# Performance work log

Measured on AMD Instinct MI355X. Metric: run time of the kernel, lower is better.

## Reference

```python
import jax, jax.numpy as jnp
import numpy as np

B, S, D = 8, 2048, 768
SCALE = jnp.sqrt(jnp.float32(D))


def setup_inputs() -> dict:
    key = jax.random.key(0)
    ks = jax.random.split(key, 9)
    sd = 1.0 / np.sqrt(D)
    return {
        "x": jax.random.normal(ks[0], (B, S, D), jnp.float32),
        "Wq": jax.random.normal(ks[1], (D, D), jnp.float32) * sd,
        "bq": jax.random.normal(ks[2], (D,), jnp.float32) * sd,
        "Wk": jax.random.normal(ks[3], (D, D), jnp.float32) * sd,
        "bk": jax.random.normal(ks[4], (D,), jnp.float32) * sd,
        "Wv": jax.random.normal(ks[5], (D, D), jnp.float32) * sd,
        "bv": jax.random.normal(ks[6], (D,), jnp.float32) * sd,
        "Wp": jax.random.normal(ks[7], (D, D), jnp.float32) * sd,
        "bp": jax.random.normal(ks[8], (D,), jnp.float32) * sd,
    }


def reference(x, Wq, bq, Wk, bk, Wv, bv, Wp, bp):
    # Linear layers: y = x @ W^T + b (torch nn.Linear convention)
    Q = jnp.einsum("bsd,ed->bse", x, Wq) + bq
    K = jnp.einsum("bsd,ed->bse", x, Wk) + bk
    V = jnp.einsum("bsd,ed->bse", x, Wv) + bv
    # Full attention matrix (no head split in original module)
    alpha = jnp.einsum("bqd,bkd->bqk", Q, K) / SCALE  # [B,S,S]
    alpha = jax.nn.softmax(alpha, axis=-1)
    # dropout is identity in eval mode
    out = jnp.einsum("bqk,bkd->bqd", alpha, V)
    out = jnp.einsum("bsd,ed->bse", out, Wp) + bp
    return out
```

## Files before the change

### kernel.cpp

```cpp
#include <hip/hip_runtime.h>
#include <stdint.h>


typedef __attribute__((ext_vector_type(8))) short short8;
typedef __attribute__((ext_vector_type(4))) float f32x4;

typedef const __attribute__((address_space(1))) void gvoid_t;
typedef __attribute__((address_space(3))) void lvoid_t;

__device__ __forceinline__ float b2f(unsigned short u) {
  union { unsigned int u; float f; } v;
  v.u = ((unsigned int)u) << 16;
  return v.f;
}
__device__ __forceinline__ unsigned short f2b(float f) {
  union { float f; unsigned int u; } v; v.f = f;
  unsigned int u = v.u;
  return (unsigned short)((u + 0x7fffu + ((u >> 16) & 1u)) >> 16);
}

struct Cvt9 {
  const void* s[9];
  unsigned short* d[9];
  long long n8[9];
  long long total8;
};

__global__ __launch_bounds__(256) void convert_inputs(Cvt9 C) {
  long long g = (long long)blockIdx.x * 256 + threadIdx.x;
  if (g >= C.total8) return;
  int s = 0;
  long long off = g;
  while (off >= C.n8[s]) { off -= C.n8[s]; ++s; }
  const float* sf = (const float*)C.s[s] + off * 8;
  unsigned short* dp = C.d[s] + off * 8;
  float4 a = ((const float4*)sf)[0];
  float4 b = ((const float4*)sf)[1];
  uint4 o;
  o.x = (unsigned int)f2b(a.x) | ((unsigned int)f2b(a.y) << 16);
  o.y = (unsigned int)f2b(a.z) | ((unsigned int)f2b(a.w) << 16);
  o.z = (unsigned int)f2b(b.x) | ((unsigned int)f2b(b.y) << 16);
  o.w = (unsigned int)f2b(b.z) | ((unsigned int)f2b(b.w) << 16);
  *(uint4*)dp = o;
}

__device__ __forceinline__ void gemm_core(
    const unsigned short* __restrict__ Ab, const unsigned short* __restrict__ Bb,
    int lda, int ldb, int K, int m0, int n0,
    unsigned short* As, unsigned short* Bs, f32x4 (&acc)[4][4])
{
  const int t    = threadIdx.x;
  const int w    = t >> 6;
  const int lane = t & 63;
  const int lo   = lane & 15;
  const int quad = lane >> 4;
  const int wr   = w >> 1;
  const int wc   = w & 1;
  const int srow  = t >> 2;
  const int sq    = ((t & 3) - ((t >> 3) & 3)) & 3;
  const int skoff = sq * 8;
  const int rq    = ((quad + (lo >> 1)) & 3) * 8;

  for (int k0 = 0; k0 < K; k0 += 64) {
#pragma unroll
    for (int c = 0; c < 2; ++c) {
#pragma unroll
      for (int r = 0; r < 2; ++r) {
        const unsigned short* ga = Ab + (size_t)(m0 + r * 64 + srow) * lda + (k0 + c * 32 + skoff);
        __builtin_amdgcn_global_load_lds((gvoid_t*)ga, (lvoid_t*)(As + c * 4096 + r * 2048 + w * 512), 16, 0, 0);
        const unsigned short* gb = Bb + (size_t)(n0 + r * 64 + srow) * ldb + (k0 + c * 32 + skoff);
        __builtin_amdgcn_global_load_lds((gvoid_t*)gb, (lvoid_t*)(Bs + c * 4096 + r * 2048 + w * 512), 16, 0, 0);
      }
    }
    __syncthreads();

#pragma unroll
    for (int c = 0; c < 2; ++c) {
      short8 af[4], bf[4];
#pragma unroll
      for (int i = 0; i < 4; ++i)
        af[i] = *(const short8*)(As + c * 4096 + wr * 2048 + (i * 16 + lo) * 32 + rq);
#pragma unroll
      for (int j = 0; j < 4; ++j)
        bf[j] = *(const short8*)(Bs + c * 4096 + wc * 2048 + (j * 16 + lo) * 32 + rq);

#pragma unroll
      for (int i = 0; i < 4; ++i)
#pragma unroll
        for (int j = 0; j < 4; ++j)
          acc[i][j] = __builtin_amdgcn_mfma_f32_16x16x32_bf16(af[i], bf[j], acc[i][j], 0, 0, 0);
    }
    __syncthreads();
  }
}

__device__ __forceinline__ void tile_to_lds(
    unsigned short* Ls, f32x4 (&acc)[4][4], int mode,
    const unsigned short* bias_n0, const float* rlrow, float scale)
{
  const int t = threadIdx.x;
  const int w = t >> 6, lane = t & 63;
  const int lo = lane & 15, quad = lane >> 4, wr = w >> 1, wc = w & 1;
#pragma unroll
  for (int j = 0; j < 4; ++j) {
    const int ct = wc * 64 + j * 16 + lo;
    const float bv = (mode == 0) ? b2f(bias_n0[ct]) : 0.f;
#pragma unroll
    for (int i = 0; i < 4; ++i) {
      const int rt = wr * 64 + i * 16 + quad * 4;
#pragma unroll
      for (int r = 0; r < 4; ++r) {
        float v = acc[i][j][r];
        if (mode == 0)      v += bv;
        else if (mode == 2) v = __expf(fminf(v * scale, 30.f));
        else                v *= __builtin_amdgcn_rcpf(rlrow[rt + r]);
        Ls[(rt + r) * 136 + ct] = f2b(v);
      }
    }
  }
  __syncthreads();
}

__device__ __forceinline__ void lds_to_global_bf16(
    const unsigned short* Ls, unsigned short* Cg, int ldc)
{
  const int t = threadIdx.x;
  const int cr = t >> 4, cc = (t & 15) * 8;
#pragma unroll
  for (int r0 = 0; r0 < 128; r0 += 16) {
    uint4 v = *(const uint4*)(Ls + (r0 + cr) * 136 + cc);
    *(uint4*)(Cg + (size_t)(r0 + cr) * ldc + cc) = v;
  }
}

__global__ __launch_bounds__(256, 2) void qkv_k(
    const unsigned short* __restrict__ xb,
    const unsigned short* __restrict__ Wq, const unsigned short* __restrict__ bq,
    const unsigned short* __restrict__ Wk, const unsigned short* __restrict__ bk,
    const unsigned short* __restrict__ Wv, const unsigned short* __restrict__ bv,
    unsigned short* __restrict__ qb, unsigned short* __restrict__ kb,
    unsigned short* __restrict__ vt)
{
  __shared__ unsigned short smem[17408];
  const int sel = blockIdx.y / 6;
  const int n0  = (blockIdx.y % 6) * 128;
  const int m0  = blockIdx.x * 128;

  const unsigned short* W;
  const unsigned short* bi;
  if (sel == 0)      { W = Wq; bi = bq; }
  else if (sel == 1) { W = Wk; bi = bk; }
  else               { W = Wv; bi = bv; }

  f32x4 acc[4][4] = {};
  gemm_core(xb, W, 768, 768, 768, m0, n0, smem, smem + 8192, acc);

  const int t = threadIdx.x;
  const int w = t >> 6, lane = t & 63;
  const int lo = lane & 15, quad = lane >> 4, wr = w >> 1, wc = w & 1;

  if (sel < 2) {
    tile_to_lds(smem, acc, 0, bi + n0, nullptr, 0.f);
    unsigned short* dst = (sel == 0) ? qb : kb;
    lds_to_global_bf16(smem, dst + (size_t)m0 * 768 + n0, 768);
    return;
  }

  unsigned short* Ls = smem;
#pragma unroll
  for (int i = 0; i < 4; ++i) {
    const int rt = wr * 64 + i * 16 + quad * 4;
#pragma unroll
    for (int j = 0; j < 4; ++j) {
      const int ct = wc * 64 + j * 16 + lo;
      const float bvv = b2f(bi[n0 + ct]);
      ushort4 pk;
      pk.x = f2b(acc[i][j][0] + bvv);
      pk.y = f2b(acc[i][j][1] + bvv);
      pk.z = f2b(acc[i][j][2] + bvv);
      pk.w = f2b(acc[i][j][3] + bvv);
      *(ushort4*)(Ls + ct * 136 + rt) = pk;
    }
  }
  __syncthreads();
  const int bb  = m0 >> 11;
  const int sin = m0 & 2047;
  unsigned short* Cb = vt + (size_t)bb * (768 * 2048);
#pragma unroll
  for (int e0 = 0; e0 < 128; e0 += 16) {
    const int et = e0 + (t >> 4);
    const int st = (t & 15) * 8;
    uint4 val = *(const uint4*)(Ls + et * 136 + st);
    *(uint4*)(Cb + (size_t)(n0 + et) * 2048 + (sin + st)) = val;
  }
}

__global__ __launch_bounds__(256, 2) void score_k(
    const unsigned short* __restrict__ Q, const unsigned short* __restrict__ Kb,
    unsigned short* __restrict__ E, float* __restrict__ rl, float scale)
{
  __shared__ unsigned short smem[17408];
  const int m0 = blockIdx.x * 128, n0 = blockIdx.y * 128, bz = blockIdx.z;

  f32x4 acc[4][4] = {};
  gemm_core(Q + (size_t)bz * 1572864, Kb + (size_t)bz * 1572864,
            768, 768, 768, m0, n0, smem, smem + 8192, acc);

  tile_to_lds(smem, acc, 2, nullptr, nullptr, scale);
  lds_to_global_bf16(smem, E + (size_t)bz * 4194304 + (size_t)m0 * 2048 + n0, 2048);

  const int t = threadIdx.x;
  const int row = t >> 1, half = t & 1;
  const unsigned short* lr = smem + row * 136 + half * 64;
  float s = 0.f;
#pragma unroll
  for (int q8 = 0; q8 < 8; ++q8) {
    uint4 v = *(const uint4*)(lr + q8 * 8);
    unsigned int uu[4] = {v.x, v.y, v.z, v.w};
#pragma unroll
    for (int c = 0; c < 4; ++c)
      s += b2f((unsigned short)(uu[c] & 0xffffu)) + b2f((unsigned short)(uu[c] >> 16));
  }
  s += __shfl_xor(s, 1);
  if (half == 0) atomicAdd(rl + bz * 2048 + m0 + row, s);
}

__global__ __launch_bounds__(256, 2) void pv_k(
    const unsigned short* __restrict__ E, const unsigned short* __restrict__ Vt,
    const float* __restrict__ rl, unsigned short* __restrict__ attn)
{
  __shared__ unsigned short smem[17408];
  const int m0 = blockIdx.x * 128, n0 = blockIdx.y * 128, bz = blockIdx.z;

  f32x4 acc[4][4] = {};
  gemm_core(E + (size_t)bz * 4194304, Vt + (size_t)bz * 1572864,
            2048, 2048, 2048, m0, n0, smem, smem + 8192, acc);

  tile_to_lds(smem, acc, 3, nullptr, rl + bz * 2048 + m0, 0.f);
  lds_to_global_bf16(smem, attn + (size_t)bz * 1572864 + (size_t)m0 * 768 + n0, 768);
}

__global__ __launch_bounds__(256, 2) void out_k(
    const unsigned short* __restrict__ attn,
    const unsigned short* __restrict__ Wp, const unsigned short* __restrict__ bp,
    float* __restrict__ Of)
{
  __shared__ unsigned short smem[17408];
  const int m0 = blockIdx.x * 128, n0 = blockIdx.y * 128;

  f32x4 acc[4][4] = {};
  gemm_core(attn, Wp, 768, 768, 768, m0, n0, smem, smem + 8192, acc);

  const int t = threadIdx.x;
  const int w = t >> 6, lane = t & 63;
  const int lo = lane & 15, quad = lane >> 4, wr = w >> 1, wc = w & 1;
  float* Lf = (float*)smem;
#pragma unroll
  for (int h = 0; h < 2; ++h) {
    __syncthreads();
    if (wc == h) {
#pragma unroll
      for (int j = 0; j < 4; ++j) {
        const int cl = j * 16 + lo;
        const float bvv = b2f(bp[n0 + h * 64 + cl]);
#pragma unroll
        for (int i = 0; i < 4; ++i) {
          const int rt = wr * 64 + i * 16 + quad * 4;
#pragma unroll
          for (int r = 0; r < 4; ++r)
            Lf[(rt + r) * 68 + cl] = acc[i][j][r] + bvv;
        }
      }
    }
    __syncthreads();
    const int cr = t >> 4, cc = (t & 15) * 4;
#pragma unroll
    for (int r0 = 0; r0 < 128; r0 += 16) {
      float4 v = *(const float4*)(Lf + (r0 + cr) * 68 + cc);
      *(float4*)(Of + (size_t)(m0 + r0 + cr) * 768 + n0 + h * 64 + cc) = v;
    }
  }
}

extern "C" void kernel_launch(void* const* d_in, const int* in_sizes, int n_in,
                              void* d_out, int out_size, void* d_ws, size_t ws_size,
                              hipStream_t stream) {
  (void)in_sizes; (void)n_in; (void)out_size; (void)ws_size;

  char* ws = (char*)d_ws;
  float* rl    = (float*)(ws + 4096);
  unsigned short* wcv = (unsigned short*)(ws + ((size_t)1 << 20));
  unsigned short* qb  = (unsigned short*)(ws + ((size_t)8  << 20));
  unsigned short* kb  = (unsigned short*)(ws + ((size_t)32 << 20));
  unsigned short* vt  = (unsigned short*)(ws + ((size_t)56 << 20));
  unsigned short* eb  = (unsigned short*)(ws + ((size_t)80 << 20));
  unsigned short* xb  = eb;
  unsigned short* attn = qb;

  unsigned short* wqb = wcv;
  unsigned short* bqb = wcv + 589824;
  unsigned short* wkb = wcv + 590592;
  unsigned short* bkb = wcv + 1180416;
  unsigned short* wvb = wcv + 1181184;
  unsigned short* bvb = wcv + 1771008;
  unsigned short* wpb = wcv + 1771776;
  unsigned short* bpb = wcv + 2361600;

  const float inv_scale = 0.036084391824351615f;
  dim3 blk(256);

  Cvt9 cv;
  cv.s[0] = d_in[0]; cv.d[0] = xb;  cv.n8[0] = 12582912 / 8;
  cv.s[1] = d_in[1]; cv.d[1] = wqb; cv.n8[1] = 589824 / 8;
  cv.s[2] = d_in[2]; cv.d[2] = bqb; cv.n8[2] = 768 / 8;
  cv.s[3] = d_in[3]; cv.d[3] = wkb; cv.n8[3] = 589824 / 8;
  cv.s[4] = d_in[4]; cv.d[4] = bkb; cv.n8[4] = 768 / 8;
  cv.s[5] = d_in[5]; cv.d[5] = wvb; cv.n8[5] = 589824 / 8;
  cv.s[6] = d_in[6]; cv.d[6] = bvb; cv.n8[6] = 768 / 8;
  cv.s[7] = d_in[7]; cv.d[7] = wpb; cv.n8[7] = 589824 / 8;
  cv.s[8] = d_in[8]; cv.d[8] = bpb; cv.n8[8] = 768 / 8;
  cv.total8 = (12582912 + 4 * (589824 + 768)) / 8;
  convert_inputs<<<(unsigned)((cv.total8 + 255) / 256), blk, 0, stream>>>(cv);

  hipMemsetAsync(rl, 0, 16384 * sizeof(float), stream);

  qkv_k<<<dim3(128, 18, 1), blk, 0, stream>>>(xb, wqb, bqb, wkb, bkb, wvb, bvb, qb, kb, vt);

  score_k<<<dim3(16, 16, 8), blk, 0, stream>>>(qb, kb, eb, rl, inv_scale);

  pv_k<<<dim3(16, 6, 8), blk, 0, stream>>>(eb, vt, rl, attn);

  out_k<<<dim3(128, 6, 1), blk, 0, stream>>>(attn, wpb, bpb, (float*)d_out);
}
```

Before: 354.7 us.

## Replace 128x128 GEMM core with double-buffered 256x256 pipelined MFMA kernel

Replaces the shared GEMM core with a 256x256-tile, 512-thread kernel. It double-buffers 64-wide K slices in LDS using XOR-swizzled direct-to-LDS loads, and interleaves prefetch of the next slices with MFMA quarter-blocks through explicit vmcnt waits, barriers and setprio. All four GEMM kernels, the epilogues and the launch grids are rewritten for the larger tile, with epilogues staged in two halves through LDS. The aim is more operand reuse per byte loaded and hiding global-load latency behind compute. In exchange it uses 128KB of LDS and many more accumulator registers per block, so occupancy drops, and the smaller grids (e.g. 192 blocks for pv_k) may leave CUs underused.

```diff
diff --git a/kernel.cpp b/kernel.cpp
--- a/kernel.cpp
+++ b/kernel.cpp
@@ -44,96 +44,147 @@
   *(uint4*)dp = o;
 }
 
-__device__ __forceinline__ void gemm_core(
-    const unsigned short* __restrict__ Ab, const unsigned short* __restrict__ Bb,
-    int lda, int ldb, int K, int m0, int n0,
-    unsigned short* As, unsigned short* Bs, f32x4 (&acc)[4][4])
+__device__ __forceinline__ void gemm256(
+    const unsigned short* __restrict__ Ag,
+    const unsigned short* __restrict__ Bg,
+    const int lda, const int ldb, const int NT,
+    unsigned short* lds, f32x4 (&acc)[8][4])
 {
   const int t    = threadIdx.x;
   const int w    = t >> 6;
   const int lane = t & 63;
   const int lo   = lane & 15;
   const int quad = lane >> 4;
-  const int wr   = w >> 1;
-  const int wc   = w & 1;
-  const int srow  = t >> 2;
-  const int sq    = ((t & 3) - ((t >> 3) & 3)) & 3;
-  const int skoff = sq * 8;
-  const int rq    = ((quad + (lo >> 1)) & 3) * 8;
-
-  for (int k0 = 0; k0 < K; k0 += 64) {
-#pragma unroll
-    for (int c = 0; c < 2; ++c) {
-#pragma unroll
-      for (int r = 0; r < 2; ++r) {
-        const unsigned short* ga = Ab + (size_t)(m0 + r * 64 + srow) * lda + (k0 + c * 32 + skoff);
-        __builtin_amdgcn_global_load_lds((gvoid_t*)ga, (lvoid_t*)(As + c * 4096 + r * 2048 + w * 512), 16, 0, 0);
-        const unsigned short* gb = Bb + (size_t)(n0 + r * 64 + srow) * ldb + (k0 + c * 32 + skoff);
-        __builtin_amdgcn_global_load_lds((gvoid_t*)gb, (lvoid_t*)(Bs + c * 4096 + r * 2048 + w * 512), 16, 0, 0);
+  const int wr   = w >> 2;
+  const int wcn  = w & 3;
+  const int swz  = ((t & 7) ^ ((t >> 3) & 7)) << 3;
+  const int wslot = w * 512;
+  const int sl0  = (quad ^ (lo & 7)) << 3;
+  const int sl1  = ((4 + quad) ^ (lo & 7)) << 3;
+  const unsigned short* pA = lds + wr * 8192 + lo * 64;
+  const unsigned short* pB = lds + 16384 + (wcn >> 1) * 8192 + ((wcn & 1) * 64 + lo) * 64;
+
+  short8 af[4][2], bf0[2][2], bf1[2][2];
+
+#define STG(gb, ld, kt, q, reg)                                                   \
+  __builtin_amdgcn_global_load_lds(                                               \
+      (gvoid_t*)((gb) + (size_t)((q) * 64 + (t >> 3)) * (ld) + (kt) * 64 + swz),  \
+      (lvoid_t*)((reg) + wslot), 16, 0, 0)
+#define SA02(kt) { unsigned short* r_ = lds + ((kt) & 1) * 32768;         \
+                   STG(Ag, lda, (kt), 0, r_); STG(Ag, lda, (kt), 2, r_ + 8192); }
+#define SA13(kt) { unsigned short* r_ = lds + ((kt) & 1) * 32768;         \
+                   STG(Ag, lda, (kt), 1, r_ + 4096); STG(Ag, lda, (kt), 3, r_ + 12288); }
+#define SB01(kt) { unsigned short* r_ = lds + ((kt) & 1) * 32768 + 16384; \
+                   STG(Bg, ldb, (kt), 0, r_); STG(Bg, ldb, (kt), 1, r_ + 4096); }
+#define SB23(kt) { unsigned short* r_ = lds + ((kt) & 1) * 32768 + 16384; \
+                   STG(Bg, ldb, (kt), 2, r_ + 8192); STG(Bg, ldb, (kt), 3, r_ + 12288); }
+#define RDA(MH, pAb) { _Pragma("unroll") for (int mi = 0; mi < 4; ++mi) {     \
+    af[mi][0] = *(const short8*)((pAb) + (MH) * 4096 + mi * 1024 + sl0);      \
+    af[mi][1] = *(const short8*)((pAb) + (MH) * 4096 + mi * 1024 + sl1); } }
+#define RDB(BF, NH, pBb) { _Pragma("unroll") for (int ni = 0; ni < 2; ++ni) { \
+    BF[ni][0] = *(const short8*)((pBb) + (NH) * 2048 + ni * 1024 + sl0);      \
+    BF[ni][1] = *(const short8*)((pBb) + (NH) * 2048 + ni * 1024 + sl1); } }
+#define MMA(MH, NH, BF) {                                                     \
+  __builtin_amdgcn_s_barrier();                                               \
+  asm volatile("s_waitcnt lgkmcnt(0)" ::: "memory");                          \
+  __builtin_amdgcn_s_setprio(1);                                              \
+  _Pragma("unroll") for (int kc = 0; kc < 2; ++kc)                            \
+  _Pragma("unroll") for (int mi = 0; mi < 4; ++mi)                            \
+  _Pragma("unroll") for (int ni = 0; ni < 2; ++ni)                            \
+    acc[(MH)*4 + mi][(NH)*2 + ni] = __builtin_amdgcn_mfma_f32_16x16x32_bf16(  \
+        af[mi][kc], BF[ni][kc], acc[(MH)*4 + mi][(NH)*2 + ni], 0, 0, 0);      \
+  __builtin_amdgcn_s_setprio(0);                                              \
+  __builtin_amdgcn_s_barrier(); }
+#define VM(n) asm volatile("s_waitcnt vmcnt(" #n ")" ::: "memory")
+
+  SA02(0); SB01(0); SA13(0); SB23(0);
+  SA02(1); SB01(1); SA13(1);
+  VM(6);
+  __builtin_amdgcn_s_barrier();
+
+  for (int kt = 0; kt < NT - 2; ++kt) {
+    const unsigned short* pAb = pA + (kt & 1) * 32768;
+    const unsigned short* pBb = pB + (kt & 1) * 32768;
+    RDA(0, pAb); RDB(bf0, 0, pBb); SB23(kt + 1);          MMA(0, 0, bf0);
+    RDB(bf1, 1, pBb);              SA02(kt + 2); VM(10);  MMA(0, 1, bf1);
+    RDA(1, pAb);                   SB01(kt + 2);          MMA(1, 0, bf0);
+                                   SA13(kt + 2); VM(6);   MMA(1, 1, bf1);
+  }
+  {
+    const int kt = NT - 2;
+    const unsigned short* pAb = pA + (kt & 1) * 32768;
+    const unsigned short* pBb = pB + (kt & 1) * 32768;
+    RDA(0, pAb); RDB(bf0, 0, pBb); SB23(kt + 1);          MMA(0, 0, bf0);
+    RDB(bf1, 1, pBb);                            VM(8);   MMA(0, 1, bf1);
+    RDA(1, pAb);                                          MMA(1, 0, bf0);
+                                                 VM(0);   MMA(1, 1, bf1);
+  }
+  {
+    const int kt = NT - 1;
+    const unsigned short* pAb = pA + (kt & 1) * 32768;
+    const unsigned short* pBb = pB + (kt & 1) * 32768;
+    RDA(0, pAb); RDB(bf0, 0, pBb);                        MMA(0, 0, bf0);
+    RDB(bf1, 1, pBb);                                     MMA(0, 1, bf1);
+    RDA(1, pAb);                                          MMA(1, 0, bf0);
+                                                          MMA(1, 1, bf1);
+  }
+#undef STG
+#undef SA02
+#undef SA13
+#undef SB01
+#undef SB23
+#undef RDA
+#undef RDB
+#undef MMA
+#undef VM
+}
+
+template<int MODE>
+__device__ __forceinline__ void epi_bf16(
+    unsigned short* Ls, f32x4 (&acc)[8][4], int h,
+    const unsigned short* bias_n0, const float* rlbase, float scale,
+    unsigned short* Cg, int ldc)
+{
+  const int t = threadIdx.x, w = t >> 6, lane = t & 63;
+  const int lo = lane & 15, quad = lane >> 4, wr = w >> 2, wcn = w & 3;
+  __syncthreads();
+  if (wr == h) {
+    float bvv[4];
+    if (MODE == 0) {
+#pragma unroll
+      for (int nf = 0; nf < 4; ++nf) bvv[nf] = b2f(bias_n0[wcn * 64 + nf * 16 + lo]);
+    }
+#pragma unroll
+    for (int mf = 0; mf < 8; ++mf) {
+      const int r0 = mf * 16 + quad * 4;
+      float rv[4];
+      if (MODE == 3) {
+#pragma unroll
+        for (int r = 0; r < 4; ++r) rv[r] = __builtin_amdgcn_rcpf(rlbase[h * 128 + r0 + r]);
       }
-    }
-    __syncthreads();
-
-#pragma unroll
-    for (int c = 0; c < 2; ++c) {
-      short8 af[4], bf[4];
-#pragma unroll
-      for (int i = 0; i < 4; ++i)
-        af[i] = *(const short8*)(As + c * 4096 + wr * 2048 + (i * 16 + lo) * 32 + rq);
-#pragma unroll
-      for (int j = 0; j < 4; ++j)
-        bf[j] = *(const short8*)(Bs + c * 4096 + wc * 2048 + (j * 16 + lo) * 32 + rq);
-
-#pragma unroll
-      for (int i = 0; i < 4; ++i)
-#pragma unroll
-        for (int j = 0; j < 4; ++j)
-          acc[i][j] = __builtin_amdgcn_mfma_f32_16x16x32_bf16(af[i], bf[j], acc[i][j], 0, 0, 0);
-    }
-    __syncthreads();
-  }
-}
-
-__device__ __forceinline__ void tile_to_lds(
-    unsigned short* Ls, f32x4 (&acc)[4][4], int mode,
-    const unsigned short* bias_n0, const float* rlrow, float scale)
-{
-  const int t = threadIdx.x;
-  const int w = t >> 6, lane = t & 63;
-  const int lo = lane & 15, quad = lane >> 4, wr = w >> 1, wc = w & 1;
-#pragma unroll
-  for (int j = 0; j < 4; ++j) {
-    const int ct = wc * 64 + j * 16 + lo;
-    const float bv = (mode == 0) ? b2f(bias_n0[ct]) : 0.f;
-#pragma unroll
-    for (int i = 0; i < 4; ++i) {
-      const int rt = wr * 64 + i * 16 + quad * 4;
-#pragma unroll
-      for (int r = 0; r < 4; ++r) {
-        float v = acc[i][j][r];
-        if (mode == 0)      v += bv;
-        else if (mode == 2) v = __expf(fminf(v * scale, 30.f));
-        else                v *= __builtin_amdgcn_rcpf(rlrow[rt + r]);
-        Ls[(rt + r) * 136 + ct] = f2b(v);
+#pragma unroll
+      for (int nf = 0; nf < 4; ++nf) {
+        const int col = wcn * 64 + nf * 16 + lo;
+#pragma unroll
+        for (int r = 0; r < 4; ++r) {
+          float v = acc[mf][nf][r];
+          if (MODE == 0)      v += bvv[nf];
+          else if (MODE == 2) v = __expf(fminf(v * scale, 30.f));
+          else if (MODE == 3) v *= rv[r];
+          Ls[(r0 + r) * 264 + col] = f2b(v);
+        }
       }
     }
   }
   __syncthreads();
-}
-
-__device__ __forceinline__ void lds_to_global_bf16(
-    const unsigned short* Ls, unsigned short* Cg, int ldc)
-{
-  const int t = threadIdx.x;
-  const int cr = t >> 4, cc = (t & 15) * 8;
-#pragma unroll
-  for (int r0 = 0; r0 < 128; r0 += 16) {
-    uint4 v = *(const uint4*)(Ls + (r0 + cr) * 136 + cc);
-    *(uint4*)(Cg + (size_t)(r0 + cr) * ldc + cc) = v;
-  }
-}
-
-__global__ __launch_bounds__(256, 2) void qkv_k(
+#pragma unroll
+  for (int u0 = 0; u0 < 8; ++u0) {
+    const int u = u0 * 512 + t, row = u >> 5, c16 = (u & 31) * 8;
+    *(uint4*)(Cg + (size_t)(h * 128 + row) * ldc + c16) = *(const uint4*)(Ls + row * 264 + c16);
+  }
+}
+
+__global__ __launch_bounds__(512, 2) void qkv_k(
     const unsigned short* __restrict__ xb,
     const unsigned short* __restrict__ Wq, const unsigned short* __restrict__ bq,
     const unsigned short* __restrict__ Wk, const unsigned short* __restrict__ bk,
@@ -141,10 +192,10 @@
     unsigned short* __restrict__ qb, unsigned short* __restrict__ kb,
     unsigned short* __restrict__ vt)
 {
-  __shared__ unsigned short smem[17408];
-  const int sel = blockIdx.y / 6;
-  const int n0  = (blockIdx.y % 6) * 128;
-  const int m0  = blockIdx.x * 128;
+  __shared__ unsigned short smem[65536];
+  const int sel = blockIdx.y / 3;
+  const int n0  = (blockIdx.y % 3) * 256;
+  const int m0  = blockIdx.x * 256;
 
   const unsigned short* W;
   const unsigned short* bi;
@@ -152,132 +203,139 @@
   else if (sel == 1) { W = Wk; bi = bk; }
   else               { W = Wv; bi = bv; }
 
-  f32x4 acc[4][4] = {};
-  gemm_core(xb, W, 768, 768, 768, m0, n0, smem, smem + 8192, acc);
-
-  const int t = threadIdx.x;
-  const int w = t >> 6, lane = t & 63;
-  const int lo = lane & 15, quad = lane >> 4, wr = w >> 1, wc = w & 1;
+  f32x4 acc[8][4] = {};
+  gemm256(xb + (size_t)m0 * 768, W + (size_t)n0 * 768, 768, 768, 12, smem, acc);
 
   if (sel < 2) {
-    tile_to_lds(smem, acc, 0, bi + n0, nullptr, 0.f);
-    unsigned short* dst = (sel == 0) ? qb : kb;
-    lds_to_global_bf16(smem, dst + (size_t)m0 * 768 + n0, 768);
+    unsigned short* dst = (sel == 0 ? qb : kb) + (size_t)m0 * 768 + n0;
+    epi_bf16<0>(smem, acc, 0, bi + n0, nullptr, 0.f, dst, 768);
+    epi_bf16<0>(smem, acc, 1, bi + n0, nullptr, 0.f, dst, 768);
     return;
   }
 
+  const int t = threadIdx.x, w = t >> 6, lane = t & 63;
+  const int lo = lane & 15, quad = lane >> 4, wr = w >> 2, wcn = w & 3;
+  const int bb2 = m0 >> 11, sin = m0 & 2047;
   unsigned short* Ls = smem;
 #pragma unroll
-  for (int i = 0; i < 4; ++i) {
-    const int rt = wr * 64 + i * 16 + quad * 4;
-#pragma unroll
-    for (int j = 0; j < 4; ++j) {
-      const int ct = wc * 64 + j * 16 + lo;
-      const float bvv = b2f(bi[n0 + ct]);
-      ushort4 pk;
-      pk.x = f2b(acc[i][j][0] + bvv);
-      pk.y = f2b(acc[i][j][1] + bvv);
-      pk.z = f2b(acc[i][j][2] + bvv);
-      pk.w = f2b(acc[i][j][3] + bvv);
-      *(ushort4*)(Ls + ct * 136 + rt) = pk;
-    }
-  }
-  __syncthreads();
-  const int bb  = m0 >> 11;
-  const int sin = m0 & 2047;
-  unsigned short* Cb = vt + (size_t)bb * (768 * 2048);
-#pragma unroll
-  for (int e0 = 0; e0 < 128; e0 += 16) {
-    const int et = e0 + (t >> 4);
-    const int st = (t & 15) * 8;
-    uint4 val = *(const uint4*)(Ls + et * 136 + st);
-    *(uint4*)(Cb + (size_t)(n0 + et) * 2048 + (sin + st)) = val;
-  }
-}
-
-__global__ __launch_bounds__(256, 2) void score_k(
+  for (int eh = 0; eh < 2; ++eh) {
+    __syncthreads();
+    if ((wcn >> 1) == eh) {
+#pragma unroll
+      for (int mf = 0; mf < 8; ++mf) {
+        const int row = wr * 128 + mf * 16 + quad * 4;
+#pragma unroll
+        for (int nf = 0; nf < 4; ++nf) {
+          const int colL = (wcn & 1) * 64 + nf * 16 + lo;
+          const float bvv = b2f(bi[n0 + eh * 128 + colL]);
+          ushort4 pk;
+          pk.x = f2b(acc[mf][nf][0] + bvv);
+          pk.y = f2b(acc[mf][nf][1] + bvv);
+          pk.z = f2b(acc[mf][nf][2] + bvv);
+          pk.w = f2b(acc[mf][nf][3] + bvv);
+          *(ushort4*)(Ls + colL * 264 + row) = pk;
+        }
+      }
+    }
+    __syncthreads();
+    unsigned short* Vb = vt + (size_t)bb2 * 1572864 + (size_t)(n0 + eh * 128) * 2048 + sin;
+#pragma unroll
+    for (int u0 = 0; u0 < 8; ++u0) {
+      const int u = u0 * 512 + t, e = u >> 5, s16 = (u & 31) * 8;
+      *(uint4*)(Vb + (size_t)e * 2048 + s16) = *(const uint4*)(Ls + e * 264 + s16);
+    }
+  }
+}
+
+__global__ __launch_bounds__(512, 2) void score_k(
     const unsigned short* __restrict__ Q, const unsigned short* __restrict__ Kb,
     unsigned short* __restrict__ E, float* __restrict__ rl, float scale)
 {
-  __shared__ unsigned short smem[17408];
-  const int m0 = blockIdx.x * 128, n0 = blockIdx.y * 128, bz = blockIdx.z;
-
-  f32x4 acc[4][4] = {};
-  gemm_core(Q + (size_t)bz * 1572864, Kb + (size_t)bz * 1572864,
-            768, 768, 768, m0, n0, smem, smem + 8192, acc);
-
-  tile_to_lds(smem, acc, 2, nullptr, nullptr, scale);
-  lds_to_global_bf16(smem, E + (size_t)bz * 4194304 + (size_t)m0 * 2048 + n0, 2048);
+  __shared__ unsigned short smem[65536];
+  const int m0 = blockIdx.x * 256, n0 = blockIdx.y * 256, bz = blockIdx.z;
+
+  f32x4 acc[8][4] = {};
+  gemm256(Q + (size_t)bz * 1572864 + (size_t)m0 * 768,
+          Kb + (size_t)bz * 1572864 + (size_t)n0 * 768, 768, 768, 12, smem, acc);
 
   const int t = threadIdx.x;
-  const int row = t >> 1, half = t & 1;
-  const unsigned short* lr = smem + row * 136 + half * 64;
-  float s = 0.f;
-#pragma unroll
-  for (int q8 = 0; q8 < 8; ++q8) {
-    uint4 v = *(const uint4*)(lr + q8 * 8);
-    unsigned int uu[4] = {v.x, v.y, v.z, v.w};
-#pragma unroll
-    for (int c = 0; c < 4; ++c)
-      s += b2f((unsigned short)(uu[c] & 0xffffu)) + b2f((unsigned short)(uu[c] >> 16));
-  }
-  s += __shfl_xor(s, 1);
-  if (half == 0) atomicAdd(rl + bz * 2048 + m0 + row, s);
-}
-
-__global__ __launch_bounds__(256, 2) void pv_k(
+  unsigned short* Eg = E + (size_t)bz * 4194304 + (size_t)m0 * 2048 + n0;
+#pragma unroll
+  for (int h = 0; h < 2; ++h) {
+    epi_bf16<2>(smem, acc, h, nullptr, nullptr, scale, Eg, 2048);
+    const int row = t >> 2, seg = t & 3;
+    const unsigned short* lr = smem + row * 264 + seg * 64;
+    float s = 0.f;
+#pragma unroll
+    for (int q8 = 0; q8 < 8; ++q8) {
+      const int qq = ((q8 + row) & 7) * 8;
+      uint4 v = *(const uint4*)(lr + qq);
+      unsigned int uu[4] = {v.x, v.y, v.z, v.w};
+#pragma unroll
+      for (int c = 0; c < 4; ++c)
+        s += b2f((unsigned short)(uu[c] & 0xffffu)) + b2f((unsigned short)(uu[c] >> 16));
+    }
+    s += __shfl_xor(s, 1);
+    s += __shfl_xor(s, 2);
+    if (seg == 0) atomicAdd(rl + bz * 2048 + m0 + h * 128 + row, s);
+  }
+}
+
+__global__ __launch_bounds__(512, 2) void pv_k(
     const unsigned short* __restrict__ E, const unsigned short* __restrict__ Vt,
     const float* __restrict__ rl, unsigned short* __restrict__ attn)
 {
-  __shared__ unsigned short smem[17408];
-  const int m0 = blockIdx.x * 128, n0 = blockIdx.y * 128, bz = blockIdx.z;
-
-  f32x4 acc[4][4] = {};
-  gemm_core(E + (size_t)bz * 4194304, Vt + (size_t)bz * 1572864,
-            2048, 2048, 2048, m0, n0, smem, smem + 8192, acc);
-
-  tile_to_lds(smem, acc, 3, nullptr, rl + bz * 2048 + m0, 0.f);
-  lds_to_global_bf16(smem, attn + (size_t)bz * 1572864 + (size_t)m0 * 768 + n0, 768);
-}
-
-__global__ __launch_bounds__(256, 2) void out_k(
+  __shared__ unsigned short smem[65536];
+  const int m0 = blockIdx.x * 256, n0 = blockIdx.y * 256, bz = blockIdx.z;
+
+  f32x4 acc[8][4] = {};
+  gemm256(E + (size_t)bz * 4194304 + (size_t)m0 * 2048,
+          Vt + (size_t)bz * 1572864 + (size_t)n0 * 2048, 2048, 2048, 32, smem, acc);
+
+  const float* rlb = rl + bz * 2048 + m0;
+  unsigned short* Cg = attn + (size_t)bz * 1572864 + (size_t)m0 * 768 + n0;
+  epi_bf16<3>(smem, acc, 0, nullptr, rlb, 0.f, Cg, 768);
+  epi_bf16<3>(smem, acc, 1, nullptr, rlb, 0.f, Cg, 768);
+}
+
+__global__ __launch_bounds__(512, 2) void out_k(
     const unsigned short* __restrict__ attn,
     const unsigned short* __restrict__ Wp, const unsigned short* __restrict__ bp,
     float* __restrict__ Of)
 {
-  __shared__ unsigned short smem[17408];
-  const int m0 = blockIdx.x * 128, n0 = blockIdx.y * 128;
-
-  f32x4 acc[4][4] = {};
-  gemm_core(attn, Wp, 768, 768, 768, m0, n0, smem, smem + 8192, acc);
-
-  const int t = threadIdx.x;
-  const int w = t >> 6, lane = t & 63;
-  const int lo = lane & 15, quad = lane >> 4, wr = w >> 1, wc = w & 1;
+  __shared__ unsigned short smem[65536];
+  const int m0 = blockIdx.x * 256, n0 = blockIdx.y * 256;
+
+  f32x4 acc[8][4] = {};
+  gemm256(attn + (size_t)m0 * 768, Wp + (size_t)n0 * 768, 768, 768, 12, smem, acc);
+
+  const int t = threadIdx.x, w = t >> 6, lane = t & 63;
+  const int lo = lane & 15, quad = lane >> 4, wr = w >> 2, wcn = w & 3;
   float* Lf = (float*)smem;
 #pragma unroll
-  for (int h = 0; h < 2; ++h) {
+  for (int p = 0; p < 4; ++p) {
     __syncthreads();
-    if (wc == h) {
-#pragma unroll
-      for (int j = 0; j < 4; ++j) {
-        const int cl = j * 16 + lo;
-        const float bvv = b2f(bp[n0 + h * 64 + cl]);
-#pragma unroll
-        for (int i = 0; i < 4; ++i) {
-          const int rt = wr * 64 + i * 16 + quad * 4;
+    if (wr == (p >> 1)) {
+#pragma unroll
+      for (int mi = 0; mi < 4; ++mi) {
+        const int mf = (p & 1) * 4 + mi;
+        const int r0 = mi * 16 + quad * 4;
+#pragma unroll
+        for (int nf = 0; nf < 4; ++nf) {
+          const int col = wcn * 64 + nf * 16 + lo;
+          const float bvv = b2f(bp[n0 + col]);
 #pragma unroll
           for (int r = 0; r < 4; ++r)
-            Lf[(rt + r) * 68 + cl] = acc[i][j][r] + bvv;
+            Lf[(r0 + r) * 264 + col] = acc[mf][nf][r] + bvv;
         }
       }
     }
     __syncthreads();
-    const int cr = t >> 4, cc = (t & 15) * 4;
-#pragma unroll
-    for (int r0 = 0; r0 < 128; r0 += 16) {
-      float4 v = *(const float4*)(Lf + (r0 + cr) * 68 + cc);
-      *(float4*)(Of + (size_t)(m0 + r0 + cr) * 768 + n0 + h * 64 + cc) = v;
+#pragma unroll
+    for (int u0 = 0; u0 < 8; ++u0) {
+      const int u = u0 * 512 + t, row = u >> 6, c4 = (u & 63) * 4;
+      *(float4*)(Of + (size_t)(m0 + p * 64 + row) * 768 + n0 + c4) =
+          *(const float4*)(Lf + row * 264 + c4);
     }
   }
 }
@@ -307,7 +365,6 @@
   unsigned short* bpb = wcv + 2361600;
 
   const float inv_scale = 0.036084391824351615f;
-  dim3 blk(256);
 
   Cvt9 cv;
   cv.s[0] = d_in[0]; cv.d[0] = xb;  cv.n8[0] = 12582912 / 8;
@@ -320,15 +377,15 @@
   cv.s[7] = d_in[7]; cv.d[7] = wpb; cv.n8[7] = 589824 / 8;
   cv.s[8] = d_in[8]; cv.d[8] = bpb; cv.n8[8] = 768 / 8;
   cv.total8 = (12582912 + 4 * (589824 + 768)) / 8;
-  convert_inputs<<<(unsigned)((cv.total8 + 255) / 256), blk, 0, stream>>>(cv);
+  convert_inputs<<<(unsigned)((cv.total8 + 255) / 256), dim3(256), 0, stream>>>(cv);
 
   hipMemsetAsync(rl, 0, 16384 * sizeof(float), stream);
 
-  qkv_k<<<dim3(128, 18, 1), blk, 0, stream>>>(xb, wqb, bqb, wkb, bkb, wvb, bvb, qb, kb, vt);
-
-  score_k<<<dim3(16, 16, 8), blk, 0, stream>>>(qb, kb, eb, rl, inv_scale);
-
-  pv_k<<<dim3(16, 6, 8), blk, 0, stream>>>(eb, vt, rl, attn);
-
-  out_k<<<dim3(128, 6, 1), blk, 0, stream>>>(attn, wpb, bpb, (float*)d_out);
-}
+  qkv_k<<<dim3(64, 9, 1), dim3(512), 0, stream>>>(xb, wqb, bqb, wkb, bkb, wvb, bvb, qb, kb, vt);
+
+  score_k<<<dim3(8, 8, 8), dim3(512), 0, stream>>>(qb, kb, eb, rl, inv_scale);
+
+  pv_k<<<dim3(8, 3, 8), dim3(512), 0, stream>>>(eb, vt, rl, attn);
+
+  out_k<<<dim3(64, 3, 1), dim3(512), 0, stream>>>(attn, wpb, bpb, (float*)d_out);
+}
```

Result: no change. 355.2 us (+0.1%).

## Double-buffer GEMM core with async LDS prefetch and half-tile epilogues

Applied to the files above, without the earlier changes.

The shared GEMM core now uses two LDS buffers with K-step 32. It prefetches the next tile through global_load_lds while MFMAs run on the current one, and uses inline ds_read_b128 with XOR swizzling and staged lgkmcnt waits. This leaves one barrier per iteration instead of two. Epilogues are rewritten to stage half or quarter tiles so LDS fits in 32KB, and launch bounds are raised to 4 blocks per CU for more occupancy. The changes add register pressure and inline asm fragility, and the smaller K step doubles the loop iterations.

```diff
diff --git a/kernel.cpp b/kernel.cpp
--- a/kernel.cpp
+++ b/kernel.cpp
@@ -44,10 +44,11 @@
   *(uint4*)dp = o;
 }
 
-__device__ __forceinline__ void gemm_core(
-    const unsigned short* __restrict__ Ab, const unsigned short* __restrict__ Bb,
-    int lda, int ldb, int K, int m0, int n0,
-    unsigned short* As, unsigned short* Bs, f32x4 (&acc)[4][4])
+__device__ __forceinline__ void gemm128(
+    const unsigned short* __restrict__ Ag,
+    const unsigned short* __restrict__ Bg,
+    const int lda, const int ldb, const int NT,
+    unsigned short* lds, f32x4 (&acc)[4][4])
 {
   const int t    = threadIdx.x;
   const int w    = t >> 6;
@@ -56,84 +57,124 @@
   const int quad = lane >> 4;
   const int wr   = w >> 1;
   const int wc   = w & 1;
-  const int srow  = t >> 2;
-  const int sq    = ((t & 3) - ((t >> 3) & 3)) & 3;
-  const int skoff = sq * 8;
-  const int rq    = ((quad + (lo >> 1)) & 3) * 8;
-
-  for (int k0 = 0; k0 < K; k0 += 64) {
-#pragma unroll
-    for (int c = 0; c < 2; ++c) {
-#pragma unroll
-      for (int r = 0; r < 2; ++r) {
-        const unsigned short* ga = Ab + (size_t)(m0 + r * 64 + srow) * lda + (k0 + c * 32 + skoff);
-        __builtin_amdgcn_global_load_lds((gvoid_t*)ga, (lvoid_t*)(As + c * 4096 + r * 2048 + w * 512), 16, 0, 0);
-        const unsigned short* gb = Bb + (size_t)(n0 + r * 64 + srow) * ldb + (k0 + c * 32 + skoff);
-        __builtin_amdgcn_global_load_lds((gvoid_t*)gb, (lvoid_t*)(Bs + c * 4096 + r * 2048 + w * 512), 16, 0, 0);
-      }
-    }
-    __syncthreads();
-
-#pragma unroll
-    for (int c = 0; c < 2; ++c) {
-      short8 af[4], bf[4];
-#pragma unroll
-      for (int i = 0; i < 4; ++i)
-        af[i] = *(const short8*)(As + c * 4096 + wr * 2048 + (i * 16 + lo) * 32 + rq);
-#pragma unroll
-      for (int j = 0; j < 4; ++j)
-        bf[j] = *(const short8*)(Bs + c * 4096 + wc * 2048 + (j * 16 + lo) * 32 + rq);
-
-#pragma unroll
-      for (int i = 0; i < 4; ++i)
-#pragma unroll
-        for (int j = 0; j < 4; ++j)
-          acc[i][j] = __builtin_amdgcn_mfma_f32_16x16x32_bf16(af[i], bf[j], acc[i][j], 0, 0, 0);
-    }
-    __syncthreads();
-  }
-}
-
-__device__ __forceinline__ void tile_to_lds(
-    unsigned short* Ls, f32x4 (&acc)[4][4], int mode,
-    const unsigned short* bias_n0, const float* rlrow, float scale)
-{
-  const int t = threadIdx.x;
-  const int w = t >> 6, lane = t & 63;
+  const int srow = t >> 2;
+  const int ssw  = ((t & 3) ^ (srow & 3)) << 3;
+
+  const unsigned lbase = (unsigned)(uintptr_t)(void*)lds;
+  const unsigned rsw   = (unsigned)((quad ^ (lo & 3)) << 4);
+  const unsigned aAr   = lbase + (unsigned)(wr * 64 + lo) * 64 + rsw;
+  const unsigned aBr   = lbase + 8192u + (unsigned)(wc * 64 + lo) * 64 + rsw;
+
+#define STG(kt, buf) {                                                              \
+  const unsigned short* a0_ = Ag + (size_t)(srow)      * lda + (kt) * 32 + ssw;     \
+  const unsigned short* a1_ = Ag + (size_t)(64 + srow) * lda + (kt) * 32 + ssw;     \
+  const unsigned short* b0_ = Bg + (size_t)(srow)      * ldb + (kt) * 32 + ssw;     \
+  const unsigned short* b1_ = Bg + (size_t)(64 + srow) * ldb + (kt) * 32 + ssw;     \
+  unsigned short* d_ = lds + (buf) * 8192 + t * 8;                                  \
+  __builtin_amdgcn_global_load_lds((gvoid_t*)a0_, (lvoid_t*)(d_),        16, 0, 0); \
+  __builtin_amdgcn_global_load_lds((gvoid_t*)a1_, (lvoid_t*)(d_ + 2048), 16, 0, 0); \
+  __builtin_amdgcn_global_load_lds((gvoid_t*)b0_, (lvoid_t*)(d_ + 4096), 16, 0, 0); \
+  __builtin_amdgcn_global_load_lds((gvoid_t*)b1_, (lvoid_t*)(d_ + 6144), 16, 0, 0); }
+#define DSR(d, a, IMM) asm volatile("ds_read_b128 %0, %1 offset:" #IMM : "=v"(d) : "v"(a))
+#define LGK(n) { asm volatile("s_waitcnt lgkmcnt(" #n ")" ::: "memory"); \
+                 __builtin_amdgcn_sched_barrier(0); }
+#define GRP(g) { _Pragma("unroll") for (int mi = 0; mi < 4; ++mi)             \
+    acc[mi][g] = __builtin_amdgcn_mfma_f32_16x16x32_bf16(                     \
+        af[mi], bf[g], acc[mi][g], 0, 0, 0); }
+
+  STG(0, 0);
+  __syncthreads();
+
+  for (int kt = 0; kt < NT; ++kt) {
+    const int buf = kt & 1;
+    if (kt + 1 < NT) STG(kt + 1, buf ^ 1);
+
+    const unsigned bo = (unsigned)(buf * 16384);
+    short8 af[4], bf[4];
+    const unsigned aA = aAr + bo, aB = aBr + bo;
+    DSR(af[0], aA, 0); DSR(af[1], aA, 1024); DSR(af[2], aA, 2048); DSR(af[3], aA, 3072);
+    DSR(bf[0], aB, 0); DSR(bf[1], aB, 1024); DSR(bf[2], aB, 2048); DSR(bf[3], aB, 3072);
+
+    __builtin_amdgcn_s_setprio(1);
+    LGK(3); GRP(0);
+    LGK(2); GRP(1);
+    LGK(1); GRP(2);
+    LGK(0); GRP(3);
+    __builtin_amdgcn_s_setprio(0);
+
+    __syncthreads();
+  }
+#undef STG
+#undef DSR
+#undef LGK
+#undef GRP
+}
+
+template<int MODE>
+__device__ __forceinline__ void epi_bf16(
+    unsigned short* Ls, f32x4 (&acc)[4][4],
+    const unsigned short* bias_n0, const float* rlbase, float scale,
+    unsigned short* Cg, int ldc, float* rlout)
+{
+  const int t = threadIdx.x, w = t >> 6, lane = t & 63;
   const int lo = lane & 15, quad = lane >> 4, wr = w >> 1, wc = w & 1;
 #pragma unroll
-  for (int j = 0; j < 4; ++j) {
-    const int ct = wc * 64 + j * 16 + lo;
-    const float bv = (mode == 0) ? b2f(bias_n0[ct]) : 0.f;
-#pragma unroll
-    for (int i = 0; i < 4; ++i) {
-      const int rt = wr * 64 + i * 16 + quad * 4;
-#pragma unroll
-      for (int r = 0; r < 4; ++r) {
-        float v = acc[i][j][r];
-        if (mode == 0)      v += bv;
-        else if (mode == 2) v = __expf(fminf(v * scale, 30.f));
-        else                v *= __builtin_amdgcn_rcpf(rlrow[rt + r]);
-        Ls[(rt + r) * 136 + ct] = f2b(v);
-      }
-    }
-  }
-  __syncthreads();
-}
-
-__device__ __forceinline__ void lds_to_global_bf16(
-    const unsigned short* Ls, unsigned short* Cg, int ldc)
-{
-  const int t = threadIdx.x;
-  const int cr = t >> 4, cc = (t & 15) * 8;
-#pragma unroll
-  for (int r0 = 0; r0 < 128; r0 += 16) {
-    uint4 v = *(const uint4*)(Ls + (r0 + cr) * 136 + cc);
-    *(uint4*)(Cg + (size_t)(r0 + cr) * ldc + cc) = v;
-  }
-}
-
-__global__ __launch_bounds__(256, 2) void qkv_k(
+  for (int h = 0; h < 2; ++h) {
+    __syncthreads();
+    if (wr == h) {
+      float bvv[4];
+      if (MODE == 0) {
+#pragma unroll
+        for (int ni = 0; ni < 4; ++ni) bvv[ni] = b2f(bias_n0[wc * 64 + ni * 16 + lo]);
+      }
+#pragma unroll
+      for (int mi = 0; mi < 4; ++mi) {
+        const int r0 = mi * 16 + quad * 4;
+        float rv[4];
+        if (MODE == 3) {
+#pragma unroll
+          for (int r = 0; r < 4; ++r) rv[r] = __builtin_amdgcn_rcpf(rlbase[h * 64 + r0 + r]);
+        }
+#pragma unroll
+        for (int ni = 0; ni < 4; ++ni) {
+          const int col = wc * 64 + ni * 16 + lo;
+#pragma unroll
+          for (int r = 0; r < 4; ++r) {
+            float v = acc[mi][ni][r];
+            if (MODE == 0)      v += bvv[ni];
+            else if (MODE == 2) v = __expf(fminf(v * scale, 30.f));
+            else if (MODE == 3) v *= rv[r];
+            Ls[(r0 + r) * 136 + col] = f2b(v);
+          }
+        }
+      }
+    }
+    __syncthreads();
+#pragma unroll
+    for (int j = 0; j < 4; ++j) {
+      const int u = j * 256 + t, row = u >> 4, c16 = (u & 15) * 8;
+      *(uint4*)(Cg + (size_t)(h * 64 + row) * ldc + c16) = *(const uint4*)(Ls + row * 136 + c16);
+    }
+    if (MODE == 2) {
+      const int row = t >> 2, seg = t & 3;
+      const unsigned short* lr = Ls + row * 136 + seg * 32;
+      float s = 0.f;
+#pragma unroll
+      for (int q4 = 0; q4 < 4; ++q4) {
+        uint4 v = *(const uint4*)(lr + q4 * 8);
+        unsigned int uu[4] = {v.x, v.y, v.z, v.w};
+#pragma unroll
+        for (int c = 0; c < 4; ++c)
+          s += b2f((unsigned short)(uu[c] & 0xffffu)) + b2f((unsigned short)(uu[c] >> 16));
+      }
+      s += __shfl_xor(s, 1);
+      s += __shfl_xor(s, 2);
+      if (seg == 0) atomicAdd(rlout + h * 64 + row, s);
+    }
+  }
+}
+
+__global__ __launch_bounds__(256, 4) void qkv_k(
     const unsigned short* __restrict__ xb,
     const unsigned short* __restrict__ Wq, const unsigned short* __restrict__ bq,
     const unsigned short* __restrict__ Wk, const unsigned short* __restrict__ bk,
@@ -141,7 +182,7 @@
     unsigned short* __restrict__ qb, unsigned short* __restrict__ kb,
     unsigned short* __restrict__ vt)
 {
-  __shared__ unsigned short smem[17408];
+  __shared__ unsigned short smem[16384];
   const int sel = blockIdx.y / 6;
   const int n0  = (blockIdx.y % 6) * 128;
   const int m0  = blockIdx.x * 128;
@@ -153,131 +194,117 @@
   else               { W = Wv; bi = bv; }
 
   f32x4 acc[4][4] = {};
-  gemm_core(xb, W, 768, 768, 768, m0, n0, smem, smem + 8192, acc);
-
-  const int t = threadIdx.x;
-  const int w = t >> 6, lane = t & 63;
+  gemm128(xb + (size_t)m0 * 768, W + (size_t)n0 * 768, 768, 768, 24, smem, acc);
+
+  if (sel < 2) {
+    unsigned short* dst = (sel == 0 ? qb : kb) + (size_t)m0 * 768 + n0;
+    epi_bf16<0>(smem, acc, bi + n0, nullptr, 0.f, dst, 768, nullptr);
+    return;
+  }
+
+  const int t = threadIdx.x, w = t >> 6, lane = t & 63;
   const int lo = lane & 15, quad = lane >> 4, wr = w >> 1, wc = w & 1;
-
-  if (sel < 2) {
-    tile_to_lds(smem, acc, 0, bi + n0, nullptr, 0.f);
-    unsigned short* dst = (sel == 0) ? qb : kb;
-    lds_to_global_bf16(smem, dst + (size_t)m0 * 768 + n0, 768);
-    return;
-  }
-
+  const int bb2 = m0 >> 11, sin = m0 & 2047;
   unsigned short* Ls = smem;
 #pragma unroll
-  for (int i = 0; i < 4; ++i) {
-    const int rt = wr * 64 + i * 16 + quad * 4;
+  for (int ec = 0; ec < 2; ++ec) {
+    __syncthreads();
+    if (wc == ec) {
+#pragma unroll
+      for (int ni = 0; ni < 4; ++ni) {
+        const int el = ni * 16 + lo;
+        const float bvv = b2f(bi[n0 + ec * 64 + el]);
+#pragma unroll
+        for (int mi = 0; mi < 4; ++mi) {
+          const int srow2 = wr * 64 + mi * 16 + quad * 4;
+          ushort4 pk;
+          pk.x = f2b(acc[mi][ni][0] + bvv);
+          pk.y = f2b(acc[mi][ni][1] + bvv);
+          pk.z = f2b(acc[mi][ni][2] + bvv);
+          pk.w = f2b(acc[mi][ni][3] + bvv);
+          *(ushort4*)(Ls + el * 136 + srow2) = pk;
+        }
+      }
+    }
+    __syncthreads();
+    unsigned short* Vb = vt + (size_t)bb2 * 1572864 + (size_t)(n0 + ec * 64) * 2048 + sin;
 #pragma unroll
     for (int j = 0; j < 4; ++j) {
-      const int ct = wc * 64 + j * 16 + lo;
-      const float bvv = b2f(bi[n0 + ct]);
-      ushort4 pk;
-      pk.x = f2b(acc[i][j][0] + bvv);
-      pk.y = f2b(acc[i][j][1] + bvv);
-      pk.z = f2b(acc[i][j][2] + bvv);
-      pk.w = f2b(acc[i][j][3] + bvv);
-      *(ushort4*)(Ls + ct * 136 + rt) = pk;
-    }
-  }
-  __syncthreads();
-  const int bb  = m0 >> 11;
-  const int sin = m0 & 2047;
-  unsigned short* Cb = vt + (size_t)bb * (768 * 2048);
-#pragma unroll
-  for (int e0 = 0; e0 < 128; e0 += 16) {
-    const int et = e0 + (t >> 4);
-    const int st = (t & 15) * 8;
-    uint4 val = *(const uint4*)(Ls + et * 136 + st);
-    *(uint4*)(Cb + (size_t)(n0 + et) * 2048 + (sin + st)) = val;
-  }
-}
-
-__global__ __launch_bounds__(256, 2) void score_k(
+      const int u = j * 256 + t, e = u >> 4, s16 = (u & 15) * 8;
+      *(uint4*)(Vb + (size_t)e * 2048 + s16) = *(const uint4*)(Ls + e * 136 + s16);
+    }
+  }
+}
+
+__global__ __launch_bounds__(256, 4) void score_k(
     const unsigned short* __restrict__ Q, const unsigned short* __restrict__ Kb,
     unsigned short* __restrict__ E, float* __restrict__ rl, float scale)
 {
-  __shared__ unsigned short smem[17408];
+  __shared__ unsigned short smem[16384];
   const int m0 = blockIdx.x * 128, n0 = blockIdx.y * 128, bz = blockIdx.z;
 
   f32x4 acc[4][4] = {};
-  gemm_core(Q + (size_t)bz * 1572864, Kb + (size_t)bz * 1572864,
-            768, 768, 768, m0, n0, smem, smem + 8192, acc);
-
-  tile_to_lds(smem, acc, 2, nullptr, nullptr, scale);
-  lds_to_global_bf16(smem, E + (size_t)bz * 4194304 + (size_t)m0 * 2048 + n0, 2048);
-
-  const int t = threadIdx.x;
-  const int row = t >> 1, half = t & 1;
-  const unsigned short* lr = smem + row * 136 + half * 64;
-  float s = 0.f;
-#pragma unroll
-  for (int q8 = 0; q8 < 8; ++q8) {
-    uint4 v = *(const uint4*)(lr + q8 * 8);
-    unsigned int uu[4] = {v.x, v.y, v.z, v.w};
-#pragma unroll
-    for (int c = 0; c < 4; ++c)
-      s += b2f((unsigned short)(uu[c] & 0xffffu)) + b2f((unsigned short)(uu[c] >> 16));
-  }
-  s += __shfl_xor(s, 1);
-  if (half == 0) atomicAdd(rl + bz * 2048 + m0 + row, s);
-}
-
-__global__ __launch_bounds__(256, 2) void pv_k(
+  gemm128(Q + (size_t)bz * 1572864 + (size_t)m0 * 768,
+          Kb + (size_t)bz * 1572864 + (size_t)n0 * 768, 768, 768, 24, smem, acc);
+
+  unsigned short* Eg = E + (size_t)bz * 4194304 + (size_t)m0 * 2048 + n0;
+  epi_bf16<2>(smem, acc, nullptr, nullptr, scale, Eg, 2048, rl + bz * 2048 + m0);
+}
+
+__global__ __launch_bounds__(256, 4) void pv_k(
     const unsigned short* __restrict__ E, const unsigned short* __restrict__ Vt,
     const float* __restrict__ rl, unsigned short* __restrict__ attn)
 {
-  __shared__ unsigned short smem[17408];
+  __shared__ unsigned short smem[16384];
   const int m0 = blockIdx.x * 128, n0 = blockIdx.y * 128, bz = blockIdx.z;
 
   f32x4 acc[4][4] = {};
-  gemm_core(E + (size_t)bz * 4194304, Vt + (size_t)bz * 1572864,
-            2048, 2048, 2048, m0, n0, smem, smem + 8192, acc);
-
-  tile_to_lds(smem, acc, 3, nullptr, rl + bz * 2048 + m0, 0.f);
-  lds_to_global_bf16(smem, attn + (size_t)bz * 1572864 + (size_t)m0 * 768 + n0, 768);
-}
-
-__global__ __launch_bounds__(256, 2) void out_k(
+  gemm128(E + (size_t)bz * 4194304 + (size_t)m0 * 2048,
+          Vt + (size_t)bz * 1572864 + (size_t)n0 * 2048, 2048, 2048, 64, smem, acc);
+
+  const float* rlb = rl + bz * 2048 + m0;
+  unsigned short* Cg = attn + (size_t)bz * 1572864 + (size_t)m0 * 768 + n0;
+  epi_bf16<3>(smem, acc, nullptr, rlb, 0.f, Cg, 768, nullptr);
+}
+
+__global__ __launch_bounds__(256, 4) void out_k(
     const unsigned short* __restrict__ attn,
     const unsigned short* __restrict__ Wp, const unsigned short* __restrict__ bp,
     float* __restrict__ Of)
 {
-  __shared__ unsigned short smem[17408];
+  __shared__ unsigned short smem[16384];
   const int m0 = blockIdx.x * 128, n0 = blockIdx.y * 128;
 
   f32x4 acc[4][4] = {};
-  gemm_core(attn, Wp, 768, 768, 768, m0, n0, smem, smem + 8192, acc);
-
-  const int t = threadIdx.x;
-  const int w = t >> 6, lane = t & 63;
+  gemm128(attn + (size_t)m0 * 768, Wp + (size_t)n0 * 768, 768, 768, 24, smem, acc);
+
+  const int t = threadIdx.x, w = t >> 6, lane = t & 63;
   const int lo = lane & 15, quad = lane >> 4, wr = w >> 1, wc = w & 1;
   float* Lf = (float*)smem;
 #pragma unroll
-  for (int h = 0; h < 2; ++h) {
-    __syncthreads();
-    if (wc == h) {
-#pragma unroll
-      for (int j = 0; j < 4; ++j) {
-        const int cl = j * 16 + lo;
-        const float bvv = b2f(bp[n0 + h * 64 + cl]);
-#pragma unroll
-        for (int i = 0; i < 4; ++i) {
-          const int rt = wr * 64 + i * 16 + quad * 4;
+  for (int p = 0; p < 4; ++p) {
+    __syncthreads();
+    if (wr == (p >> 1)) {
+#pragma unroll
+      for (int mm = 0; mm < 2; ++mm) {
+        const int mi = (p & 1) * 2 + mm;
+        const int lr0 = mm * 16 + quad * 4;
+#pragma unroll
+        for (int ni = 0; ni < 4; ++ni) {
+          const int col = wc * 64 + ni * 16 + lo;
+          const float bvv = b2f(bp[n0 + col]);
 #pragma unroll
           for (int r = 0; r < 4; ++r)
-            Lf[(rt + r) * 68 + cl] = acc[i][j][r] + bvv;
+            Lf[(lr0 + r) * 132 + col] = acc[mi][ni][r] + bvv;
         }
       }
     }
     __syncthreads();
-    const int cr = t >> 4, cc = (t & 15) * 4;
-#pragma unroll
-    for (int r0 = 0; r0 < 128; r0 += 16) {
-      float4 v = *(const float4*)(Lf + (r0 + cr) * 68 + cc);
-      *(float4*)(Of + (size_t)(m0 + r0 + cr) * 768 + n0 + h * 64 + cc) = v;
+#pragma unroll
+    for (int j = 0; j < 4; ++j) {
+      const int u = j * 256 + t, row = u >> 5, c4 = (u & 31) * 4;
+      *(float4*)(Of + (size_t)(m0 + p * 32 + row) * 768 + n0 + c4) =
+          *(const float4*)(Lf + row * 132 + c4);
     }
   }
 }
@@ -307,7 +334,6 @@
   unsigned short* bpb = wcv + 2361600;
 
   const float inv_scale = 0.036084391824351615f;
-  dim3 blk(256);
 
   Cvt9 cv;
   cv.s[0] = d_in[0]; cv.d[0] = xb;  cv.n8[0] = 12582912 / 8;
@@ -320,15 +346,15 @@
   cv.s[7] = d_in[7]; cv.d[7] = wpb; cv.n8[7] = 589824 / 8;
   cv.s[8] = d_in[8]; cv.d[8] = bpb; cv.n8[8] = 768 / 8;
   cv.total8 = (12582912 + 4 * (589824 + 768)) / 8;
-  convert_inputs<<<(unsigned)((cv.total8 + 255) / 256), blk, 0, stream>>>(cv);
+  convert_inputs<<<(unsigned)((cv.total8 + 255) / 256), dim3(256), 0, stream>>>(cv);
 
   hipMemsetAsync(rl, 0, 16384 * sizeof(float), stream);
 
-  qkv_k<<<dim3(128, 18, 1), blk, 0, stream>>>(xb, wqb, bqb, wkb, bkb, wvb, bvb, qb, kb, vt);
-
-  score_k<<<dim3(16, 16, 8), blk, 0, stream>>>(qb, kb, eb, rl, inv_scale);
-
-  pv_k<<<dim3(16, 6, 8), blk, 0, stream>>>(eb, vt, rl, attn);
-
-  out_k<<<dim3(128, 6, 1), blk, 0, stream>>>(attn, wpb, bpb, (float*)d_out);
-}
+  qkv_k<<<dim3(128, 18, 1), dim3(256), 0, stream>>>(xb, wqb, bqb, wkb, bkb, wvb, bvb, qb, kb, vt);
+
+  score_k<<<dim3(16, 16, 8), dim3(256), 0, stream>>>(qb, kb, eb, rl, inv_scale);
+
+  pv_k<<<dim3(16, 6, 8), dim3(256), 0, stream>>>(eb, vt, rl, attn);
+
+  out_k<<<dim3(128, 6, 1), dim3(256), 0, stream>>>(attn, wpb, bpb, (float*)d_out);
+}
```

Result: no change. 352.1 us (-0.7%).
